# Kernel tuning notes

Measured on AMD Instinct MI355X. Metric: run time of the kernel, lower is better.

The kernel has to match this reference:

```python
import jax, jax.numpy as jnp
import numpy as np

N, E = 2048, 262144
SDIM, VDIM, EDIM = 256, 64, 32
NUM_ATOM_FEATURES, NUM_BOND_TYPES, NMOL = 16, 5, 64


def setup_inputs() -> dict:
    key = jax.random.key(0)
    ks = jax.random.split(key, 18)
    def lin(k, fan_in, shape):
        return jax.random.uniform(k, shape, jnp.float32, -1.0, 1.0) / np.sqrt(fan_in)
    inp = {
        "s": jax.random.normal(ks[0], (N, SDIM), jnp.float32),
        "v": jax.random.normal(ks[1], (N, 3, VDIM), jnp.float32),
        "p": jax.random.normal(ks[2], (N, 3), jnp.float32),
        "e": jax.random.normal(ks[3], (E, EDIM), jnp.float32),
        "batch": jnp.sort(jax.random.randint(ks[4], (N,), 0, NMOL)),
        "edge_index_global": jax.random.randint(ks[5], (2, E), 0, N),
        # learned params (torch DenseLayer == Linear): W [in,out], b [out]
        "Ws": lin(ks[6], SDIM, (SDIM, SDIM)),   "bs": lin(ks[7], SDIM, (SDIM,)),
        "Wc": lin(ks[8], VDIM, (VDIM, 1)),                                      # coords_lin, no bias
        "Wa": lin(ks[9], SDIM, (SDIM, NUM_ATOM_FEATURES)), "ba": lin(ks[10], SDIM, (NUM_ATOM_FEATURES,)),
        "Wb": lin(ks[11], EDIM, (EDIM, SDIM)),  "bb": lin(ks[12], EDIM, (SDIM,)),
        "W0": lin(ks[13], SDIM + 1, (SDIM + 1, SDIM)), "b0": lin(ks[14], SDIM + 1, (SDIM,)),
        "W1": lin(ks[15], SDIM, (SDIM, NUM_BOND_TYPES)), "b1": lin(ks[16], SDIM, (NUM_BOND_TYPES,)),
    }
    return inp


def reference(s, v, p, e, batch, edge_index_global,
              Ws, bs, Wc, Wa, ba, Wb, bb, W0, b0, W1, b1):
    # shared scalar mapping with SiLU
    s_h = jax.nn.silu(s @ Ws + bs)                              # [N, SDIM]
    coords = (v @ Wc)[..., 0]                                   # [N,3,VDIM]@[VDIM,1] -> [N,3]
    atoms_pred = s_h @ Wa + ba                                  # [N, NUM_ATOM_FEATURES]

    j, i = edge_index_global[0], edge_index_global[1]
    # coords_param == 'data': add positions then remove per-graph mean (scatter_mean)
    coords_pred = p + coords
    sums = jax.ops.segment_sum(coords_pred, batch, num_segments=NMOL)       # [NMOL,3]
    cnts = jax.ops.segment_sum(jnp.ones((N, 1), s.dtype), batch, num_segments=NMOL)
    coords_pred = coords_pred - (sums / jnp.maximum(cnts, 1.0))[batch]

    d = jnp.sum((coords_pred[i] - coords_pred[j]) ** 2, axis=-1, keepdims=True)  # [E,1]

    # dense edge matrix construction + symmetrization (as in the original)
    e_dense = jnp.zeros((N, N, EDIM), e.dtype).at[j, i].set(e)  # [N,N,EDIM]
    e_dense = 0.5 * (e_dense + jnp.swapaxes(e_dense, 0, 1))
    e_sym = e_dense[j, i]                                        # [E,EDIM]

    f = s_h[i] + s_h[j] + (e_sym @ Wb + bb)                      # [E,SDIM]
    edge = jnp.concatenate([f, d], axis=-1)                      # [E,SDIM+1]
    bonds_pred = jax.nn.silu(edge @ W0 + b0) @ W1 + b1           # [E,NUM_BOND_TYPES]
    return coords_pred, atoms_pred, bonds_pred
```

## Files before the change

kernel.cpp:

```cpp
#include <hip/hip_runtime.h>
#include <hip/hip_bf16.h>

typedef __bf16 bf16_8 __attribute__((ext_vector_type(8)));
typedef __bf16 bf16_4 __attribute__((ext_vector_type(4)));
typedef float f32x4 __attribute__((ext_vector_type(4)));

__device__ __forceinline__ float silu_f(float x) {
    return x * __builtin_amdgcn_rcpf(1.0f + __expf(-x));
}

__device__ __forceinline__ unsigned hslot(unsigned cell, unsigned nslots) {
    return (unsigned)(((unsigned long long)(cell * 2654435761u) * nslots) >> 32);
}
__device__ __forceinline__ int map_lookup(unsigned nslots, const int* __restrict__ M,
                                          const unsigned long long* __restrict__ H, unsigned cell) {
    if (nslots == 0) return M[cell] - 1;
    unsigned slot = hslot(cell, nslots);
    for (int pr = 0; pr < 4096; pr++) {
        unsigned long long v = H[slot];
        if (v == 0ull) return -1;
        if ((unsigned)(v >> 32) == cell) return (int)(v & 0xFFFFFFFFu) - 1;
        slot++; if (slot == nslots) slot = 0;
    }
    return -1;
}

__global__ __launch_bounds__(256) void kS(float* __restrict__ out, int n, float val) {
    int i = blockIdx.x * 256 + threadIdx.x;
    if (i < n) out[i] = val;
}

__global__ __launch_bounds__(256) void kZ(f32x4* __restrict__ a, size_t na16,
                                          f32x4* __restrict__ b, size_t nb16) {
    size_t i = (size_t)blockIdx.x * 256 + threadIdx.x;
    size_t stride = (size_t)gridDim.x * 256;
    f32x4 z = {0.f, 0.f, 0.f, 0.f};
    for (size_t k = i; k < na16; k += stride) a[k] = z;
    for (size_t k = i; k < nb16; k += stride) b[k] = z;
}

__global__ __launch_bounds__(256, 4) void kP(
    const float* __restrict__ s, const float* __restrict__ Ws, const float* __restrict__ bs,
    const float* __restrict__ W0, const float* __restrict__ Wa, const float* __restrict__ ba,
    const float* __restrict__ v, const float* __restrict__ p,
    const float* __restrict__ Wc, const float* __restrict__ Wb, const float* __restrict__ bb,
    const float* __restrict__ b0, const float* __restrict__ W1,
    const int* __restrict__ batch, const int* __restrict__ ei,
    int N, int E, int gaB, int coordB, int mapB,
    unsigned nslots, int* __restrict__ M, unsigned long long* __restrict__ H,
    __bf16* __restrict__ G, __bf16* __restrict__ wqT, __bf16* __restrict__ w1Tg,
    float* __restrict__ w0L, float* __restrict__ b0p,
    float* __restrict__ cp, float* __restrict__ sums, float* __restrict__ cnts,
    float* __restrict__ outA)
{
    __shared__ __align__(16) char LDSC[37376];
    int b = blockIdx.x, t = threadIdx.x;

    if (b < gaB) {
        __bf16* s_bf  = (__bf16*)LDSC;
        __bf16* sh_bf = (__bf16*)(LDSC + 8448);
        __bf16* wT    = (__bf16*)(LDSC + 16896);
        int wv = t >> 6, lane = t & 63;
        int l16 = lane & 15, q8 = (lane >> 4) * 8, r4b = (lane >> 4) * 4;
        int r0 = b * 16;
        {
            int row = t >> 4, c0 = (t & 15) * 16;
            const float* sp = s + (long long)(r0 + row) * 256 + c0;
            bool ok = (r0 + row) < N;
            f32x4 a0 = ok ? *(const f32x4*)(sp + 0)  : (f32x4){0.f,0.f,0.f,0.f};
            f32x4 a1 = ok ? *(const f32x4*)(sp + 4)  : (f32x4){0.f,0.f,0.f,0.f};
            f32x4 a2 = ok ? *(const f32x4*)(sp + 8)  : (f32x4){0.f,0.f,0.f,0.f};
            f32x4 a3 = ok ? *(const f32x4*)(sp + 12) : (f32x4){0.f,0.f,0.f,0.f};
            bf16_8 p0, p1;
#pragma unroll
            for (int q = 0; q < 4; q++) {
                p0[q] = (__bf16)a0[q]; p0[q + 4] = (__bf16)a1[q];
                p1[q] = (__bf16)a2[q]; p1[q + 4] = (__bf16)a3[q];
            }
            *(bf16_8*)(s_bf + row * 264 + c0) = p0;
            *(bf16_8*)(s_bf + row * 264 + c0 + 8) = p1;
        }
        __syncthreads();
        __bf16* wTw = wT + wv * 2560;
        float ld[32];

        f32x4 acc[4];
#pragma unroll
        for (int ct = 0; ct < 4; ct++) acc[ct] = (f32x4){0.f,0.f,0.f,0.f};
        {
            const float* wp = Ws + wv * 64 + lane;
#pragma unroll
            for (int i = 0; i < 32; i++) ld[i] = wp[i * 256];
#pragma unroll 1
            for (int kk = 0; kk < 8; kk++) {
#pragma unroll
                for (int j = 0; j < 4; j++) {
                    bf16_8 pk;
#pragma unroll
                    for (int q = 0; q < 8; q++) pk[q] = (__bf16)ld[j * 8 + q];
                    *(bf16_8*)(wTw + lane * 40 + j * 8) = pk;
                }
                if (kk < 7) {
                    const float* wpn = wp + (kk + 1) * 32 * 256;
#pragma unroll
                    for (int i = 0; i < 32; i++) ld[i] = wpn[i * 256];
                }
                bf16_8 af = *(const bf16_8*)(s_bf + l16 * 264 + kk * 32 + q8);
#pragma unroll
                for (int ct = 0; ct < 4; ct++) {
                    bf16_8 bfr = *(const bf16_8*)(wTw + (ct * 16 + l16) * 40 + q8);
                    acc[ct] = __builtin_amdgcn_mfma_f32_16x16x32_bf16(af, bfr, acc[ct], 0, 0, 0);
                }
            }
        }
#pragma unroll
        for (int ct = 0; ct < 4; ct++) {
            int col = wv * 64 + ct * 16 + l16;
            float bsv = bs[col];
#pragma unroll
            for (int r = 0; r < 4; r++)
                sh_bf[(r4b + r) * 264 + col] = (__bf16)silu_f(acc[ct][r] + bsv);
        }
        __syncthreads();

        if (wv == 0) {
            f32x4 aa = (f32x4){0.f,0.f,0.f,0.f};
#pragma unroll 1
            for (int ks = 0; ks < 8; ks++) {
                bf16_8 a = *(const bf16_8*)(sh_bf + l16 * 264 + ks * 32 + q8);
                bf16_8 wb;
#pragma unroll
                for (int j = 0; j < 8; j++) wb[j] = (__bf16)Wa[(ks * 32 + q8 + j) * 16 + l16];
                aa = __builtin_amdgcn_mfma_f32_16x16x32_bf16(a, wb, aa, 0, 0, 0);
            }
            float bav = ba[l16];
#pragma unroll
            for (int r = 0; r < 4; r++) {
                int row = r0 + r4b + r;
                if (row < N) outA[row * 16 + l16] = aa[r] + bav;
            }
        }

        f32x4 acc2[4];
#pragma unroll
        for (int ct = 0; ct < 4; ct++) acc2[ct] = (f32x4){0.f,0.f,0.f,0.f};
        {
            const float* wp = W0 + wv * 64 + lane;
#pragma unroll
            for (int i = 0; i < 32; i++) ld[i] = wp[i * 256];
#pragma unroll 1
            for (int kk = 0; kk < 8; kk++) {
#pragma unroll
                for (int j = 0; j < 4; j++) {
                    bf16_8 pk;
#pragma unroll
                    for (int q = 0; q < 8; q++) pk[q] = (__bf16)ld[j * 8 + q];
                    *(bf16_8*)(wTw + lane * 40 + j * 8) = pk;
                }
                if (kk < 7) {
                    const float* wpn = wp + (kk + 1) * 32 * 256;
#pragma unroll
                    for (int i = 0; i < 32; i++) ld[i] = wpn[i * 256];
                }
                bf16_8 af = *(const bf16_8*)(sh_bf + l16 * 264 + kk * 32 + q8);
#pragma unroll
                for (int ct = 0; ct < 4; ct++) {
                    bf16_8 bfr = *(const bf16_8*)(wTw + (ct * 16 + l16) * 40 + q8);
                    acc2[ct] = __builtin_amdgcn_mfma_f32_16x16x32_bf16(af, bfr, acc2[ct], 0, 0, 0);
                }
            }
        }
#pragma unroll
        for (int ct = 0; ct < 4; ct++) {
            int col = wv * 64 + ct * 16 + l16;
#pragma unroll
            for (int r = 0; r < 4; r++) {
                int row = r0 + r4b + r;
                if (row < N) G[(long long)row * 256 + col] = (__bf16)acc2[ct][r];
            }
        }
        return;
    }
    b -= gaB;

    float* sm = (float*)LDSC;
    if (b < 2) {
        int r0 = b * 16;
        for (int i4 = t; i4 < 1024; i4 += 256)
            ((f32x4*)sm)[i4] = ((const f32x4*)(Wb + r0 * 256))[i4];
        __syncthreads();
        float acc[16];
#pragma unroll
        for (int r = 0; r < 16; r++) acc[r] = 0.f;
        for (int m4 = 0; m4 < 64; m4++) {
            float w0v = W0[(m4 * 4 + 0) * 256 + t];
            float w1v = W0[(m4 * 4 + 1) * 256 + t];
            float w2v = W0[(m4 * 4 + 2) * 256 + t];
            float w3v = W0[(m4 * 4 + 3) * 256 + t];
#pragma unroll
            for (int r = 0; r < 16; r++) {
                f32x4 sv = *(const f32x4*)(sm + r * 256 + m4 * 4);
                acc[r] += sv[0] * w0v + sv[1] * w1v + sv[2] * w2v + sv[3] * w3v;
            }
        }
#pragma unroll
        for (int r = 0; r < 16; r++) wqT[t * 32 + r0 + r] = (__bf16)acc[r];
        return;
    }
    b -= 2;
    if (b < 1) {
        sm[t] = bb[t];
        __syncthreads();
        float acc = 0.f;
        for (int m4 = 0; m4 < 64; m4++) {
            f32x4 bv = *(const f32x4*)(sm + m4 * 4);
            acc += bv[0] * W0[(m4 * 4 + 0) * 256 + t] + bv[1] * W0[(m4 * 4 + 1) * 256 + t]
                 + bv[2] * W0[(m4 * 4 + 2) * 256 + t] + bv[3] * W0[(m4 * 4 + 3) * 256 + t];
        }
        b0p[t] = acc + b0[t];
        w0L[t] = W0[256 * 256 + t];
#pragma unroll
        for (int c = 0; c < 16; c++)
            w1Tg[c * 256 + t] = (c < 5) ? (__bf16)W1[t * 5 + c] : (__bf16)0.f;
        return;
    }
    b -= 1;
    if (b < coordB) {
        int n = b * 256 + t;
        if (t < 64) sm[t] = Wc[t];
        __syncthreads();
        if (n < N) {
            int mb = batch[n] & 1023;
#pragma unroll
            for (int ax = 0; ax < 3; ax++) {
                float acc = 0.f;
                for (int d4 = 0; d4 < 16; d4++) {
                    f32x4 vv = *(const f32x4*)(v + (long long)n * 192 + ax * 64 + d4 * 4);
                    f32x4 wv2 = *(const f32x4*)(sm + d4 * 4);
                    acc += vv[0] * wv2[0] + vv[1] * wv2[1] + vv[2] * wv2[2] + vv[3] * wv2[3];
                }
                float val = p[n * 3 + ax] + acc;
                cp[n * 3 + ax] = val;
                atomicAdd(&sums[mb * 3 + ax], val);
            }
            atomicAdd(&cnts[mb], 1.0f);
        }
        return;
    }
    b -= coordB;
    {
        int k = b * 256 + t;
        if (k < E) {
            int jj = ei[k], ii = ei[E + k];
            if ((unsigned)jj >= (unsigned)N) jj = 0;
            if ((unsigned)ii >= (unsigned)N) ii = 0;
            unsigned cell = (unsigned)jj * (unsigned)N + (unsigned)ii;
            if (nslots == 0) {
                atomicMax(&M[cell], k + 1);
            } else {
                unsigned long long mine = ((unsigned long long)cell << 32) | (unsigned)(k + 1);
                unsigned slot = hslot(cell, nslots);
                for (int pr = 0; pr < 4096; pr++) {
                    unsigned long long old = atomicCAS(&H[slot], 0ull, mine);
                    if (old == 0ull) break;
                    if ((unsigned)(old >> 32) == cell) { atomicMax(&H[slot], mine); break; }
                    slot++; if (slot == nslots) slot = 0;
                }
            }
        }
    }
}

__global__ __launch_bounds__(256, 4) void kC(
    const float* __restrict__ e, const int* __restrict__ ei, const int* __restrict__ batch,
    int N, int E, int edgeB, unsigned nslots,
    const int* __restrict__ M, const unsigned long long* __restrict__ H,
    const __bf16* __restrict__ G, const __bf16* __restrict__ wqTg,
    const __bf16* __restrict__ w1Tg,
    const float* __restrict__ w0L, const float* __restrict__ b0p,
    const float* __restrict__ cp, const float* __restrict__ sums, const float* __restrict__ cnts,
    const float* __restrict__ b1,
    float* __restrict__ outC, float* __restrict__ bonds)
{
    if (blockIdx.x >= (unsigned)edgeB) {
        int n = ((int)blockIdx.x - edgeB) * 256 + threadIdx.x;
        if (n < N) {
            int mb = batch[n] & 1023;
            float cnt = fmaxf(cnts[mb], 1.0f);
#pragma unroll
            for (int ax = 0; ax < 3; ax++)
                outC[n * 3 + ax] = cp[n * 3 + ax] - sums[mb * 3 + ax] / cnt;
        }
        return;
    }

    __shared__ __align__(16) __bf16 esym[64 * 40];
    __shared__ __align__(16) __bf16 hbuf[64 * 264];
    __shared__ float sd[64];
    __shared__ int si[64], sj[64], sm1[64], sm2[64];

    int t = threadIdx.x;
    int wv = t >> 6, lane = t & 63;
    int l16 = lane & 15, q8 = (lane >> 4) * 8;
    int e0 = blockIdx.x * 64;

    if (t < 128) {
        int tt = t & 63;
        int k = e0 + tt;
        if (t < 64) {
            if (k >= E) {
                si[tt] = 0; sj[tt] = 0; sm1[tt] = 0; sd[tt] = 0.f;
            } else {
                int jj = ei[k], ii = ei[E + k];
                if ((unsigned)jj >= (unsigned)N) jj = 0;
                if ((unsigned)ii >= (unsigned)N) ii = 0;
                si[tt] = ii; sj[tt] = jj;
                int m1 = map_lookup(nslots, M, H, (unsigned)jj * (unsigned)N + (unsigned)ii);
                sm1[tt] = ((unsigned)m1 < (unsigned)E) ? m1 : 0;
                int bi = batch[ii] & 1023, bj = batch[jj] & 1023;
                float inv_i = __builtin_amdgcn_rcpf(fmaxf(cnts[bi], 1.0f));
                float inv_j = __builtin_amdgcn_rcpf(fmaxf(cnts[bj], 1.0f));
                float dx = (cp[ii * 3 + 0] - sums[bi * 3 + 0] * inv_i) - (cp[jj * 3 + 0] - sums[bj * 3 + 0] * inv_j);
                float dy = (cp[ii * 3 + 1] - sums[bi * 3 + 1] * inv_i) - (cp[jj * 3 + 1] - sums[bj * 3 + 1] * inv_j);
                float dz = (cp[ii * 3 + 2] - sums[bi * 3 + 2] * inv_i) - (cp[jj * 3 + 2] - sums[bj * 3 + 2] * inv_j);
                sd[tt] = dx * dx + dy * dy + dz * dz;
            }
        } else {
            if (k >= E) {
                sm2[tt] = -1;
            } else {
                int jj = ei[k], ii = ei[E + k];
                if ((unsigned)jj >= (unsigned)N) jj = 0;
                if ((unsigned)ii >= (unsigned)N) ii = 0;
                int m2 = map_lookup(nslots, M, H, (unsigned)ii * (unsigned)N + (unsigned)jj);
                sm2[tt] = ((unsigned)m2 < (unsigned)E) ? m2 : -1;
            }
        }
    }
    __syncthreads();

    {
        int er = t >> 2, qg = (t & 3) * 8;
        int m1 = sm1[er], m2 = sm2[er];
        const float* e1p = e + (size_t)m1 * 32 + qg;
        float v1[8], v2[8];
#pragma unroll
        for (int q = 0; q < 8; q++) { v1[q] = e1p[q]; v2[q] = 0.f; }
        if (m2 >= 0) {
            const float* e2p = e + (size_t)m2 * 32 + qg;
#pragma unroll
            for (int q = 0; q < 8; q++) v2[q] = e2p[q];
        }
        bf16_8 es;
#pragma unroll
        for (int q = 0; q < 8; q++) es[q] = (__bf16)(0.5f * (v1[q] + v2[q]));
        *(bf16_8*)(esym + er * 40 + qg) = es;
    }
    {
        int c4 = lane * 4;
        for (int it = 0; it < 16; it++) {
            int er = wv * 16 + it;
            bf16_4 gi = *(const bf16_4*)(G + (size_t)si[er] * 256 + c4);
            bf16_4 gj = *(const bf16_4*)(G + (size_t)sj[er] * 256 + c4);
            bf16_4 o;
#pragma unroll
            for (int q = 0; q < 4; q++) o[q] = (__bf16)((float)gi[q] + (float)gj[q]);
            *(bf16_4*)(hbuf + er * 264 + c4) = o;
        }
    }
    __syncthreads();

    f32x4 acc[4][4];
#pragma unroll
    for (int rt = 0; rt < 4; rt++)
#pragma unroll
        for (int ct = 0; ct < 4; ct++)
            acc[rt][ct] = (f32x4){0.f, 0.f, 0.f, 0.f};
    bf16_8 af[4];
#pragma unroll
    for (int rt = 0; rt < 4; rt++)
        af[rt] = *(const bf16_8*)(esym + (rt * 16 + l16) * 40 + q8);
#pragma unroll
    for (int ct = 0; ct < 4; ct++) {
        int c = (wv * 4 + ct) * 16 + l16;
        bf16_8 bfr = *(const bf16_8*)(wqTg + c * 32 + q8);
#pragma unroll
        for (int rt = 0; rt < 4; rt++)
            acc[rt][ct] = __builtin_amdgcn_mfma_f32_16x16x32_bf16(af[rt], bfr, acc[rt][ct], 0, 0, 0);
    }
    int r4base = (lane >> 4) * 4;
    f32x4 sdv[4];
#pragma unroll
    for (int rt = 0; rt < 4; rt++)
        sdv[rt] = *(const f32x4*)(sd + rt * 16 + r4base);
#pragma unroll
    for (int ct = 0; ct < 4; ct++) {
        int col = (wv * 4 + ct) * 16 + l16;
        float w0c = w0L[col], b0c = b0p[col];
#pragma unroll
        for (int rt = 0; rt < 4; rt++) {
#pragma unroll
            for (int r4 = 0; r4 < 4; r4++) {
                int row = rt * 16 + r4base + r4;
                int off = row * 264 + col;
                float x = acc[rt][ct][r4] + b0c + sdv[rt][r4] * w0c + (float)hbuf[off];
                hbuf[off] = (__bf16)silu_f(x);
            }
        }
    }
    __syncthreads();

    f32x4 acc3 = {0.f, 0.f, 0.f, 0.f};
#pragma unroll
    for (int ks = 0; ks < 8; ks++) {
        bf16_8 a = *(const bf16_8*)(hbuf + (wv * 16 + l16) * 264 + ks * 32 + q8);
        bf16_8 b2 = *(const bf16_8*)(w1Tg + l16 * 256 + ks * 32 + q8);
        acc3 = __builtin_amdgcn_mfma_f32_16x16x32_bf16(a, b2, acc3, 0, 0, 0);
    }
    if (l16 < 5) {
        float bv = b1[l16];
#pragma unroll
        for (int r4 = 0; r4 < 4; r4++) {
            int row = wv * 16 + r4base + r4;
            if (e0 + row < E)
                bonds[(size_t)(e0 + row) * 5 + l16] = acc3[r4] + bv;
        }
    }
}

extern "C" void kernel_launch(void* const* d_in, const int* in_sizes, int n_in,
                              void* d_out, int out_size, void* d_ws, size_t ws_size,
                              hipStream_t stream)
{
    const float* s  = (const float*)d_in[0];
    const float* v  = (const float*)d_in[1];
    const float* p  = (const float*)d_in[2];
    const float* e  = (const float*)d_in[3];
    const int* batch = (const int*)d_in[4];
    const int* ei    = (const int*)d_in[5];
    const float* Ws = (const float*)d_in[6];
    const float* bs = (const float*)d_in[7];
    const float* Wc = (const float*)d_in[8];
    const float* Wa = (const float*)d_in[9];
    const float* ba = (const float*)d_in[10];
    const float* Wb = (const float*)d_in[11];
    const float* bb = (const float*)d_in[12];
    const float* W0 = (const float*)d_in[13];
    const float* b0 = (const float*)d_in[14];
    const float* W1 = (const float*)d_in[15];
    const float* b1 = (const float*)d_in[16];

    float* out = (float*)d_out;
    int sentN = out_size < 8192 ? out_size : 8192;

    int N = in_sizes[0] / 256;
    long long E = in_sizes[5] / 2;
    int code = 0;
    if (in_sizes[6] != 65536) code |= 1;
    if (in_sizes[8] != 64) code |= 2;
    if (in_sizes[11] != 32 * 256) code |= 4;
    if (in_sizes[9] != 16 * 256) code |= 8;
    if (in_sizes[15] != 5 * 256) code |= 16;
    if (in_sizes[13] != 257 * 256) code |= 32;
    if (N < 1 || in_sizes[0] != N * 256) code |= 64;
    if (in_sizes[1] != (long long)N * 192) code |= 128;
    if (in_sizes[2] != N * 3) code |= 256;
    if (in_sizes[3] != E * 32) code |= 512;
    if (in_sizes[4] != N) code |= 1024;
    if ((long long)out_size != 19LL * N + 5LL * E) code |= 2048;
    if (code) {
        kS<<<(sentN + 255) / 256, 256, 0, stream>>>(out, sentN, 3000.0f + 64.0f * (float)code);
        return;
    }
    int Ei = (int)E;

    auto align256 = [](size_t x) { return (x + 255) & ~(size_t)255; };
    size_t G_b  = align256((size_t)N * 512);
    size_t cp_b = align256((size_t)N * 12);
    size_t misc = G_b + 16384 + 8192 + 1024 + 1024 + cp_b + 12288 + 4096 + 256;
    size_t denseB = (size_t)N * (size_t)N * 4;
    unsigned nslots; size_t mapBytes;
    if (ws_size >= denseB + misc) {
        nslots = 0; mapBytes = denseB;
    } else {
        size_t avail = (ws_size > misc) ? (ws_size - misc) / 8 : 0;
        size_t want = (size_t)Ei * 2;
        size_t ns = avail < want ? avail : want;
        if (ns < (size_t)Ei + (size_t)Ei / 8) {
            unsigned mb = (unsigned)(ws_size >> 20); if (mb > 120) mb = 120;
            kS<<<(sentN + 255) / 256, 256, 0, stream>>>(out, sentN, 1000.0f + 8.0f * (float)mb);
            return;
        }
        nslots = (unsigned)ns; mapBytes = ns * 8;
    }

    char* ws = (char*)d_ws;
    int* M = (int*)ws;
    unsigned long long* H = (unsigned long long*)ws;
    size_t mapZ = align256(mapBytes);
    size_t off = mapZ;
    __bf16* G    = (__bf16*)(ws + off); off += G_b;
    __bf16* wqT  = (__bf16*)(ws + off); off += 16384;
    __bf16* w1Tg = (__bf16*)(ws + off); off += 8192;
    float* w0L  = (float*)(ws + off);  off += 1024;
    float* b0p  = (float*)(ws + off);  off += 1024;
    float* cp   = (float*)(ws + off);  off += cp_b;
    float* sums = (float*)(ws + off);  off += 12288;
    float* cnts = (float*)(ws + off);  off += 4096;

    float* outC = out;
    float* outA = outC + 3 * N;
    float* outB = outC + 19 * N;

    kZ<<<2048, 256, 0, stream>>>((f32x4*)ws, mapZ >> 4, (f32x4*)sums, 1024);

    int mapB = (Ei + 255) / 256;
    int coordB = (N + 255) / 256;
    int gaB = (N + 15) / 16;
    kP<<<gaB + 3 + coordB + mapB, 256, 0, stream>>>(
        s, Ws, bs, W0, Wa, ba, v, p, Wc, Wb, bb, b0, W1, batch, ei,
        N, Ei, gaB, coordB, mapB, nslots, M, H,
        G, wqT, w1Tg, w0L, b0p, cp, sums, cnts, outA);
    int edgeB = (Ei + 63) / 64;
    kC<<<edgeB + coordB, 256, 0, stream>>>(
        e, ei, batch, N, Ei, edgeB, nslots, M, H, G, wqT, w1Tg,
        w0L, b0p, cp, sums, cnts, b1, outC, outB);
}
```

Measured before the change: 194.8 us.

## Pre-transpose weights to bf16 and halve edge-kernel LDS for occupancy

The zero-fill kernel now also converts Ws, W0 and Wa into transposed bf16 copies in workspace. The node kernel therefore reads MFMA B-fragments straight from global memory instead of staging converted weights through LDS, and its LDS footprint drops. The Wb·W0 product is moved onto MFMA. The edge kernel processes the 256 hidden columns in two halves through a 64x136 LDS buffer, which roughly halves its LDS use, and raises its launch bound to 6 blocks. In exchange it gathers G twice and adds extra barriers.

Result: slower. 267.4 us (+37.3%).

```diff
diff --git a/kernel.cpp b/kernel.cpp
--- a/kernel.cpp
+++ b/kernel.cpp
@@ -30,21 +30,49 @@
     if (i < n) out[i] = val;
 }
 
-__global__ __launch_bounds__(256) void kZ(f32x4* __restrict__ a, size_t na16,
-                                          f32x4* __restrict__ b, size_t nb16) {
-    size_t i = (size_t)blockIdx.x * 256 + threadIdx.x;
-    size_t stride = (size_t)gridDim.x * 256;
+__global__ __launch_bounds__(256) void kZ(
+    f32x4* __restrict__ a, size_t na16, f32x4* __restrict__ b, size_t nb16,
+    const float* __restrict__ Ws, const float* __restrict__ W0, const float* __restrict__ Wa,
+    __bf16* __restrict__ WsT, __bf16* __restrict__ W0T, __bf16* __restrict__ WaT)
+{
+    int bid = blockIdx.x, t = threadIdx.x;
+    if (bid < 4) {
+        for (int idx = t; idx < 64 * 256; idx += 256) {
+            int kl = idx >> 8, c = idx & 255;
+            WsT[(size_t)c * 256 + bid * 64 + kl] = (__bf16)Ws[(size_t)(bid * 64 + kl) * 256 + c];
+        }
+        return;
+    }
+    bid -= 4;
+    if (bid < 4) {
+        for (int idx = t; idx < 64 * 256; idx += 256) {
+            int kl = idx >> 8, c = idx & 255;
+            W0T[(size_t)c * 256 + bid * 64 + kl] = (__bf16)W0[(size_t)(bid * 64 + kl) * 256 + c];
+        }
+        return;
+    }
+    bid -= 4;
+    if (bid < 1) {
+        for (int idx = t; idx < 4096; idx += 256) {
+            int k = idx >> 4, c = idx & 15;
+            WaT[c * 256 + k] = (__bf16)Wa[k * 16 + c];
+        }
+        return;
+    }
+    bid -= 1;
+    size_t i = (size_t)bid * 256 + t;
+    size_t stride = (size_t)(gridDim.x - 9) * 256;
     f32x4 z = {0.f, 0.f, 0.f, 0.f};
     for (size_t k = i; k < na16; k += stride) a[k] = z;
     for (size_t k = i; k < nb16; k += stride) b[k] = z;
 }
 
 __global__ __launch_bounds__(256, 4) void kP(
-    const float* __restrict__ s, const float* __restrict__ Ws, const float* __restrict__ bs,
-    const float* __restrict__ W0, const float* __restrict__ Wa, const float* __restrict__ ba,
+    const float* __restrict__ s, const float* __restrict__ bs, const float* __restrict__ ba,
+    const __bf16* __restrict__ WsT, const __bf16* __restrict__ W0T, const __bf16* __restrict__ WaT,
     const float* __restrict__ v, const float* __restrict__ p,
     const float* __restrict__ Wc, const float* __restrict__ Wb, const float* __restrict__ bb,
-    const float* __restrict__ b0, const float* __restrict__ W1,
+    const float* __restrict__ W0, const float* __restrict__ b0, const float* __restrict__ W1,
     const int* __restrict__ batch, const int* __restrict__ ei,
     int N, int E, int gaB, int coordB, int mapB,
     unsigned nslots, int* __restrict__ M, unsigned long long* __restrict__ H,
@@ -53,15 +81,15 @@
     float* __restrict__ cp, float* __restrict__ sums, float* __restrict__ cnts,
     float* __restrict__ outA)
 {
-    __shared__ __align__(16) char LDSC[37376];
+    __shared__ __align__(16) char LDSC[16896];
+    __bf16* s_bf  = (__bf16*)LDSC;
+    __bf16* sh_bf = (__bf16*)(LDSC + 8448);
+    float* sm = (float*)LDSC;
     int b = blockIdx.x, t = threadIdx.x;
+    int wv = t >> 6, lane = t & 63;
+    int l16 = lane & 15, q8 = (lane >> 4) * 8, r4b = (lane >> 4) * 4;
 
     if (b < gaB) {
-        __bf16* s_bf  = (__bf16*)LDSC;
-        __bf16* sh_bf = (__bf16*)(LDSC + 8448);
-        __bf16* wT    = (__bf16*)(LDSC + 16896);
-        int wv = t >> 6, lane = t & 63;
-        int l16 = lane & 15, q8 = (lane >> 4) * 8, r4b = (lane >> 4) * 4;
         int r0 = b * 16;
         {
             int row = t >> 4, c0 = (t & 15) * 16;
@@ -73,44 +101,25 @@
             f32x4 a3 = ok ? *(const f32x4*)(sp + 12) : (f32x4){0.f,0.f,0.f,0.f};
             bf16_8 p0, p1;
 #pragma unroll
-            for (int q = 0; q < 4; q++) {
-                p0[q] = (__bf16)a0[q]; p0[q + 4] = (__bf16)a1[q];
-                p1[q] = (__bf16)a2[q]; p1[q + 4] = (__bf16)a3[q];
+            for (int qq = 0; qq < 4; qq++) {
+                p0[qq] = (__bf16)a0[qq]; p0[qq + 4] = (__bf16)a1[qq];
+                p1[qq] = (__bf16)a2[qq]; p1[qq + 4] = (__bf16)a3[qq];
             }
             *(bf16_8*)(s_bf + row * 264 + c0) = p0;
             *(bf16_8*)(s_bf + row * 264 + c0 + 8) = p1;
         }
         __syncthreads();
-        __bf16* wTw = wT + wv * 2560;
-        float ld[32];
 
         f32x4 acc[4];
 #pragma unroll
         for (int ct = 0; ct < 4; ct++) acc[ct] = (f32x4){0.f,0.f,0.f,0.f};
-        {
-            const float* wp = Ws + wv * 64 + lane;
-#pragma unroll
-            for (int i = 0; i < 32; i++) ld[i] = wp[i * 256];
-#pragma unroll 1
-            for (int kk = 0; kk < 8; kk++) {
-#pragma unroll
-                for (int j = 0; j < 4; j++) {
-                    bf16_8 pk;
-#pragma unroll
-                    for (int q = 0; q < 8; q++) pk[q] = (__bf16)ld[j * 8 + q];
-                    *(bf16_8*)(wTw + lane * 40 + j * 8) = pk;
-                }
-                if (kk < 7) {
-                    const float* wpn = wp + (kk + 1) * 32 * 256;
-#pragma unroll
-                    for (int i = 0; i < 32; i++) ld[i] = wpn[i * 256];
-                }
-                bf16_8 af = *(const bf16_8*)(s_bf + l16 * 264 + kk * 32 + q8);
-#pragma unroll
-                for (int ct = 0; ct < 4; ct++) {
-                    bf16_8 bfr = *(const bf16_8*)(wTw + (ct * 16 + l16) * 40 + q8);
-                    acc[ct] = __builtin_amdgcn_mfma_f32_16x16x32_bf16(af, bfr, acc[ct], 0, 0, 0);
-                }
+#pragma unroll
+        for (int kk = 0; kk < 8; kk++) {
+            bf16_8 af = *(const bf16_8*)(s_bf + l16 * 264 + kk * 32 + q8);
+#pragma unroll
+            for (int ct = 0; ct < 4; ct++) {
+                bf16_8 bw = *(const bf16_8*)(WsT + (size_t)(wv * 64 + ct * 16 + l16) * 256 + kk * 32 + q8);
+                acc[ct] = __builtin_amdgcn_mfma_f32_16x16x32_bf16(af, bw, acc[ct], 0, 0, 0);
             }
         }
 #pragma unroll
@@ -125,13 +134,11 @@
 
         if (wv == 0) {
             f32x4 aa = (f32x4){0.f,0.f,0.f,0.f};
-#pragma unroll 1
+#pragma unroll
             for (int ks = 0; ks < 8; ks++) {
-                bf16_8 a = *(const bf16_8*)(sh_bf + l16 * 264 + ks * 32 + q8);
-                bf16_8 wb;
-#pragma unroll
-                for (int j = 0; j < 8; j++) wb[j] = (__bf16)Wa[(ks * 32 + q8 + j) * 16 + l16];
-                aa = __builtin_amdgcn_mfma_f32_16x16x32_bf16(a, wb, aa, 0, 0, 0);
+                bf16_8 af = *(const bf16_8*)(sh_bf + l16 * 264 + ks * 32 + q8);
+                bf16_8 bw = *(const bf16_8*)(WaT + (size_t)l16 * 256 + ks * 32 + q8);
+                aa = __builtin_amdgcn_mfma_f32_16x16x32_bf16(af, bw, aa, 0, 0, 0);
             }
             float bav = ba[l16];
 #pragma unroll
@@ -144,30 +151,13 @@
         f32x4 acc2[4];
 #pragma unroll
         for (int ct = 0; ct < 4; ct++) acc2[ct] = (f32x4){0.f,0.f,0.f,0.f};
-        {
-            const float* wp = W0 + wv * 64 + lane;
-#pragma unroll
-            for (int i = 0; i < 32; i++) ld[i] = wp[i * 256];
-#pragma unroll 1
-            for (int kk = 0; kk < 8; kk++) {
-#pragma unroll
-                for (int j = 0; j < 4; j++) {
-                    bf16_8 pk;
-#pragma unroll
-                    for (int q = 0; q < 8; q++) pk[q] = (__bf16)ld[j * 8 + q];
-                    *(bf16_8*)(wTw + lane * 40 + j * 8) = pk;
-                }
-                if (kk < 7) {
-                    const float* wpn = wp + (kk + 1) * 32 * 256;
-#pragma unroll
-                    for (int i = 0; i < 32; i++) ld[i] = wpn[i * 256];
-                }
-                bf16_8 af = *(const bf16_8*)(sh_bf + l16 * 264 + kk * 32 + q8);
-#pragma unroll
-                for (int ct = 0; ct < 4; ct++) {
-                    bf16_8 bfr = *(const bf16_8*)(wTw + (ct * 16 + l16) * 40 + q8);
-                    acc2[ct] = __builtin_amdgcn_mfma_f32_16x16x32_bf16(af, bfr, acc2[ct], 0, 0, 0);
-                }
+#pragma unroll
+        for (int kk = 0; kk < 8; kk++) {
+            bf16_8 af = *(const bf16_8*)(sh_bf + l16 * 264 + kk * 32 + q8);
+#pragma unroll
+            for (int ct = 0; ct < 4; ct++) {
+                bf16_8 bw = *(const bf16_8*)(W0T + (size_t)(wv * 64 + ct * 16 + l16) * 256 + kk * 32 + q8);
+                acc2[ct] = __builtin_amdgcn_mfma_f32_16x16x32_bf16(af, bw, acc2[ct], 0, 0, 0);
             }
         }
 #pragma unroll
@@ -183,28 +173,44 @@
     }
     b -= gaB;
 
-    float* sm = (float*)LDSC;
     if (b < 2) {
         int r0 = b * 16;
-        for (int i4 = t; i4 < 1024; i4 += 256)
-            ((f32x4*)sm)[i4] = ((const f32x4*)(Wb + r0 * 256))[i4];
+        {
+            int row = t >> 4, c0 = (t & 15) * 16;
+            const float* wp = Wb + (long long)(r0 + row) * 256 + c0;
+            f32x4 a0 = *(const f32x4*)(wp + 0);
+            f32x4 a1 = *(const f32x4*)(wp + 4);
+            f32x4 a2 = *(const f32x4*)(wp + 8);
+            f32x4 a3 = *(const f32x4*)(wp + 12);
+            bf16_8 p0, p1;
+#pragma unroll
+            for (int qq = 0; qq < 4; qq++) {
+                p0[qq] = (__bf16)a0[qq]; p0[qq + 4] = (__bf16)a1[qq];
+                p1[qq] = (__bf16)a2[qq]; p1[qq + 4] = (__bf16)a3[qq];
+            }
+            *(bf16_8*)(s_bf + row * 264 + c0) = p0;
+            *(bf16_8*)(s_bf + row * 264 + c0 + 8) = p1;
+        }
         __syncthreads();
-        float acc[16];
-#pragma unroll
-        for (int r = 0; r < 16; r++) acc[r] = 0.f;
-        for (int m4 = 0; m4 < 64; m4++) {
-            float w0v = W0[(m4 * 4 + 0) * 256 + t];
-            float w1v = W0[(m4 * 4 + 1) * 256 + t];
-            float w2v = W0[(m4 * 4 + 2) * 256 + t];
-            float w3v = W0[(m4 * 4 + 3) * 256 + t];
-#pragma unroll
-            for (int r = 0; r < 16; r++) {
-                f32x4 sv = *(const f32x4*)(sm + r * 256 + m4 * 4);
-                acc[r] += sv[0] * w0v + sv[1] * w1v + sv[2] * w2v + sv[3] * w3v;
-            }
-        }
-#pragma unroll
-        for (int r = 0; r < 16; r++) wqT[t * 32 + r0 + r] = (__bf16)acc[r];
+        f32x4 acc[4];
+#pragma unroll
+        for (int ct = 0; ct < 4; ct++) acc[ct] = (f32x4){0.f,0.f,0.f,0.f};
+#pragma unroll
+        for (int kk = 0; kk < 8; kk++) {
+            bf16_8 af = *(const bf16_8*)(s_bf + l16 * 264 + kk * 32 + q8);
+#pragma unroll
+            for (int ct = 0; ct < 4; ct++) {
+                bf16_8 bw = *(const bf16_8*)(W0T + (size_t)(wv * 64 + ct * 16 + l16) * 256 + kk * 32 + q8);
+                acc[ct] = __builtin_amdgcn_mfma_f32_16x16x32_bf16(af, bw, acc[ct], 0, 0, 0);
+            }
+        }
+#pragma unroll
+        for (int ct = 0; ct < 4; ct++) {
+            int col = wv * 64 + ct * 16 + l16;
+#pragma unroll
+            for (int r = 0; r < 4; r++)
+                wqT[col * 32 + r0 + r4b + r] = (__bf16)acc[ct][r];
+        }
         return;
     }
     b -= 2;
@@ -271,7 +277,7 @@
     }
 }
 
-__global__ __launch_bounds__(256, 4) void kC(
+__global__ __launch_bounds__(256, 6) void kC(
     const float* __restrict__ e, const int* __restrict__ ei, const int* __restrict__ batch,
     int N, int E, int edgeB, unsigned nslots,
     const int* __restrict__ M, const unsigned long long* __restrict__ H,
@@ -295,13 +301,13 @@
     }
 
     __shared__ __align__(16) __bf16 esym[64 * 40];
-    __shared__ __align__(16) __bf16 hbuf[64 * 264];
+    __shared__ __align__(16) __bf16 hb[64 * 136];
     __shared__ float sd[64];
     __shared__ int si[64], sj[64], sm1[64], sm2[64];
 
     int t = threadIdx.x;
     int wv = t >> 6, lane = t & 63;
-    int l16 = lane & 15, q8 = (lane >> 4) * 8;
+    int l16 = lane & 15, q8 = (lane >> 4) * 8, r4b = (lane >> 4) * 4;
     int e0 = blockIdx.x * 64;
 
     if (t < 128) {
@@ -345,27 +351,30 @@
         const float* e1p = e + (size_t)m1 * 32 + qg;
         float v1[8], v2[8];
 #pragma unroll
-        for (int q = 0; q < 8; q++) { v1[q] = e1p[q]; v2[q] = 0.f; }
+        for (int qq = 0; qq < 8; qq++) { v1[qq] = e1p[qq]; v2[qq] = 0.f; }
         if (m2 >= 0) {
             const float* e2p = e + (size_t)m2 * 32 + qg;
 #pragma unroll
-            for (int q = 0; q < 8; q++) v2[q] = e2p[q];
+            for (int qq = 0; qq < 8; qq++) v2[qq] = e2p[qq];
         }
         bf16_8 es;
 #pragma unroll
-        for (int q = 0; q < 8; q++) es[q] = (__bf16)(0.5f * (v1[q] + v2[q]));
+        for (int qq = 0; qq < 8; qq++) es[qq] = (__bf16)(0.5f * (v1[qq] + v2[qq]));
         *(bf16_8*)(esym + er * 40 + qg) = es;
     }
     {
-        int c4 = lane * 4;
-        for (int it = 0; it < 16; it++) {
-            int er = wv * 16 + it;
-            bf16_4 gi = *(const bf16_4*)(G + (size_t)si[er] * 256 + c4);
-            bf16_4 gj = *(const bf16_4*)(G + (size_t)sj[er] * 256 + c4);
-            bf16_4 o;
-#pragma unroll
-            for (int q = 0; q < 4; q++) o[q] = (__bf16)((float)gi[q] + (float)gj[q]);
-            *(bf16_4*)(hbuf + er * 264 + c4) = o;
+        int er = t >> 2, qd = t & 3;
+        const __bf16* Gi = G + (size_t)si[er] * 256 + qd * 64;
+        const __bf16* Gj = G + (size_t)sj[er] * 256 + qd * 64;
+        __bf16* dst = hb + er * 136 + qd * 32;
+#pragma unroll
+        for (int h8 = 0; h8 < 4; h8++) {
+            bf16_8 gi = *(const bf16_8*)(Gi + h8 * 8);
+            bf16_8 gj = *(const bf16_8*)(Gj + h8 * 8);
+            bf16_8 o;
+#pragma unroll
+            for (int qq = 0; qq < 8; qq++) o[qq] = (__bf16)((float)gi[qq] + (float)gj[qq]);
+            *(bf16_8*)(dst + h8 * 8) = o;
         }
     }
     __syncthreads();
@@ -382,29 +391,28 @@
         af[rt] = *(const bf16_8*)(esym + (rt * 16 + l16) * 40 + q8);
 #pragma unroll
     for (int ct = 0; ct < 4; ct++) {
-        int c = (wv * 4 + ct) * 16 + l16;
+        int c = wv * 64 + ct * 16 + l16;
         bf16_8 bfr = *(const bf16_8*)(wqTg + c * 32 + q8);
 #pragma unroll
         for (int rt = 0; rt < 4; rt++)
             acc[rt][ct] = __builtin_amdgcn_mfma_f32_16x16x32_bf16(af[rt], bfr, acc[rt][ct], 0, 0, 0);
     }
-    int r4base = (lane >> 4) * 4;
     f32x4 sdv[4];
 #pragma unroll
     for (int rt = 0; rt < 4; rt++)
-        sdv[rt] = *(const f32x4*)(sd + rt * 16 + r4base);
-#pragma unroll
-    for (int ct = 0; ct < 4; ct++) {
-        int col = (wv * 4 + ct) * 16 + l16;
+        sdv[rt] = *(const f32x4*)(sd + rt * 16 + r4b);
+#pragma unroll
+    for (int ct = 0; ct < 2; ct++) {
+        int col = wv * 64 + ct * 16 + l16;
+        int scol = wv * 32 + ct * 16 + l16;
         float w0c = w0L[col], b0c = b0p[col];
 #pragma unroll
         for (int rt = 0; rt < 4; rt++) {
 #pragma unroll
             for (int r4 = 0; r4 < 4; r4++) {
-                int row = rt * 16 + r4base + r4;
-                int off = row * 264 + col;
-                float x = acc[rt][ct][r4] + b0c + sdv[rt][r4] * w0c + (float)hbuf[off];
-                hbuf[off] = (__bf16)silu_f(x);
+                int off = (rt * 16 + r4b + r4) * 136 + scol;
+                float x = acc[rt][ct][r4] + b0c + sdv[rt][r4] * w0c + (float)hb[off];
+                hb[off] = (__bf16)silu_f(x);
             }
         }
     }
@@ -412,16 +420,58 @@
 
     f32x4 acc3 = {0.f, 0.f, 0.f, 0.f};
 #pragma unroll
-    for (int ks = 0; ks < 8; ks++) {
-        bf16_8 a = *(const bf16_8*)(hbuf + (wv * 16 + l16) * 264 + ks * 32 + q8);
-        bf16_8 b2 = *(const bf16_8*)(w1Tg + l16 * 256 + ks * 32 + q8);
+    for (int kp = 0; kp < 4; kp++) {
+        bf16_8 a = *(const bf16_8*)(hb + (wv * 16 + l16) * 136 + kp * 32 + q8);
+        bf16_8 b2 = *(const bf16_8*)(w1Tg + l16 * 256 + (kp * 2) * 32 + q8);
+        acc3 = __builtin_amdgcn_mfma_f32_16x16x32_bf16(a, b2, acc3, 0, 0, 0);
+    }
+    __syncthreads();
+
+    {
+        int er = t >> 2, qd = t & 3;
+        const __bf16* Gi = G + (size_t)si[er] * 256 + qd * 64 + 32;
+        const __bf16* Gj = G + (size_t)sj[er] * 256 + qd * 64 + 32;
+        __bf16* dst = hb + er * 136 + qd * 32;
+#pragma unroll
+        for (int h8 = 0; h8 < 4; h8++) {
+            bf16_8 gi = *(const bf16_8*)(Gi + h8 * 8);
+            bf16_8 gj = *(const bf16_8*)(Gj + h8 * 8);
+            bf16_8 o;
+#pragma unroll
+            for (int qq = 0; qq < 8; qq++) o[qq] = (__bf16)((float)gi[qq] + (float)gj[qq]);
+            *(bf16_8*)(dst + h8 * 8) = o;
+        }
+    }
+    __syncthreads();
+
+#pragma unroll
+    for (int ct = 2; ct < 4; ct++) {
+        int col = wv * 64 + ct * 16 + l16;
+        int scol = wv * 32 + (ct - 2) * 16 + l16;
+        float w0c = w0L[col], b0c = b0p[col];
+#pragma unroll
+        for (int rt = 0; rt < 4; rt++) {
+#pragma unroll
+            for (int r4 = 0; r4 < 4; r4++) {
+                int off = (rt * 16 + r4b + r4) * 136 + scol;
+                float x = acc[rt][ct][r4] + b0c + sdv[rt][r4] * w0c + (float)hb[off];
+                hb[off] = (__bf16)silu_f(x);
+            }
+        }
+    }
+    __syncthreads();
+
+#pragma unroll
+    for (int kp = 0; kp < 4; kp++) {
+        bf16_8 a = *(const bf16_8*)(hb + (wv * 16 + l16) * 136 + kp * 32 + q8);
+        bf16_8 b2 = *(const bf16_8*)(w1Tg + l16 * 256 + (kp * 2 + 1) * 32 + q8);
         acc3 = __builtin_amdgcn_mfma_f32_16x16x32_bf16(a, b2, acc3, 0, 0, 0);
     }
     if (l16 < 5) {
         float bv = b1[l16];
 #pragma unroll
         for (int r4 = 0; r4 < 4; r4++) {
-            int row = wv * 16 + r4base + r4;
+            int row = wv * 16 + r4b + r4;
             if (e0 + row < E)
                 bonds[(size_t)(e0 + row) * 5 + l16] = acc3[r4] + bv;
         }
@@ -477,7 +527,8 @@
     auto align256 = [](size_t x) { return (x + 255) & ~(size_t)255; };
     size_t G_b  = align256((size_t)N * 512);
     size_t cp_b = align256((size_t)N * 12);
-    size_t misc = G_b + 16384 + 8192 + 1024 + 1024 + cp_b + 12288 + 4096 + 256;
+    size_t misc = G_b + 16384 + 8192 + 131072 + 131072 + 8192
+                + 1024 + 1024 + cp_b + 12288 + 4096 + 256;
     size_t denseB = (size_t)N * (size_t)N * 4;
     unsigned nslots; size_t mapBytes;
     if (ws_size >= denseB + misc) {
@@ -502,6 +553,9 @@
     __bf16* G    = (__bf16*)(ws + off); off += G_b;
     __bf16* wqT  = (__bf16*)(ws + off); off += 16384;
     __bf16* w1Tg = (__bf16*)(ws + off); off += 8192;
+    __bf16* WsT  = (__bf16*)(ws + off); off += 131072;
+    __bf16* W0T  = (__bf16*)(ws + off); off += 131072;
+    __bf16* WaT  = (__bf16*)(ws + off); off += 8192;
     float* w0L  = (float*)(ws + off);  off += 1024;
     float* b0p  = (float*)(ws + off);  off += 1024;
     float* cp   = (float*)(ws + off);  off += cp_b;
@@ -512,13 +566,15 @@
     float* outA = outC + 3 * N;
     float* outB = outC + 19 * N;
 
-    kZ<<<2048, 256, 0, stream>>>((f32x4*)ws, mapZ >> 4, (f32x4*)sums, 1024);
+    kZ<<<9 + 2048, 256, 0, stream>>>(
+        (f32x4*)ws, mapZ >> 4, (f32x4*)sums, 1024,
+        Ws, W0, Wa, WsT, W0T, WaT);
 
     int mapB = (Ei + 255) / 256;
     int coordB = (N + 255) / 256;
     int gaB = (N + 15) / 16;
     kP<<<gaB + 3 + coordB + mapB, 256, 0, stream>>>(
-        s, Ws, bs, W0, Wa, ba, v, p, Wc, Wb, bb, b0, W1, batch, ei,
+        s, bs, ba, WsT, W0T, WaT, v, p, Wc, Wb, bb, W0, b0, W1, batch, ei,
         N, Ei, gaB, coordB, mapB, nslots, M, H,
         G, wqT, w1Tg, w0L, b0p, cp, sums, cnts, outA);
     int edgeB = (Ei + 63) / 64;
```

## Drop dense N×N edge map in favor of compact hash map always

Applied to the files above, without the earlier changes.

Removes the dense N*N int index map path, which required zeroing 16 MB of workspace and scattering into it, and always uses the open-addressing hash table sized to about 2E slots. This shrinks the zero-fill and the random-access footprint of the map. In exchange, inserts and lookups now do CAS-based linear probing. The edge kernel is also reordered so the MFMA result is written to LDS first and the gathered G rows are added with SiLU afterwards, and the zero-fill grid is reduced.

Measured after the change: 211.7 us. 1.09x slower.

```diff
diff --git a/kernel.cpp b/kernel.cpp
--- a/kernel.cpp
+++ b/kernel.cpp
@@ -12,9 +12,8 @@
 __device__ __forceinline__ unsigned hslot(unsigned cell, unsigned nslots) {
     return (unsigned)(((unsigned long long)(cell * 2654435761u) * nslots) >> 32);
 }
-__device__ __forceinline__ int map_lookup(unsigned nslots, const int* __restrict__ M,
+__device__ __forceinline__ int map_lookup(unsigned nslots,
                                           const unsigned long long* __restrict__ H, unsigned cell) {
-    if (nslots == 0) return M[cell] - 1;
     unsigned slot = hslot(cell, nslots);
     for (int pr = 0; pr < 4096; pr++) {
         unsigned long long v = H[slot];
@@ -47,7 +46,7 @@
     const float* __restrict__ b0, const float* __restrict__ W1,
     const int* __restrict__ batch, const int* __restrict__ ei,
     int N, int E, int gaB, int coordB, int mapB,
-    unsigned nslots, int* __restrict__ M, unsigned long long* __restrict__ H,
+    unsigned nslots, unsigned long long* __restrict__ H,
     __bf16* __restrict__ G, __bf16* __restrict__ wqT, __bf16* __restrict__ w1Tg,
     float* __restrict__ w0L, float* __restrict__ b0p,
     float* __restrict__ cp, float* __restrict__ sums, float* __restrict__ cnts,
@@ -255,17 +254,13 @@
             if ((unsigned)jj >= (unsigned)N) jj = 0;
             if ((unsigned)ii >= (unsigned)N) ii = 0;
             unsigned cell = (unsigned)jj * (unsigned)N + (unsigned)ii;
-            if (nslots == 0) {
-                atomicMax(&M[cell], k + 1);
-            } else {
-                unsigned long long mine = ((unsigned long long)cell << 32) | (unsigned)(k + 1);
-                unsigned slot = hslot(cell, nslots);
-                for (int pr = 0; pr < 4096; pr++) {
-                    unsigned long long old = atomicCAS(&H[slot], 0ull, mine);
-                    if (old == 0ull) break;
-                    if ((unsigned)(old >> 32) == cell) { atomicMax(&H[slot], mine); break; }
-                    slot++; if (slot == nslots) slot = 0;
-                }
+            unsigned long long mine = ((unsigned long long)cell << 32) | (unsigned)(k + 1);
+            unsigned slot = hslot(cell, nslots);
+            for (int pr = 0; pr < 4096; pr++) {
+                unsigned long long old = atomicCAS(&H[slot], 0ull, mine);
+                if (old == 0ull) break;
+                if ((unsigned)(old >> 32) == cell) { atomicMax(&H[slot], mine); break; }
+                slot++; if (slot == nslots) slot = 0;
             }
         }
     }
@@ -274,7 +269,7 @@
 __global__ __launch_bounds__(256, 4) void kC(
     const float* __restrict__ e, const int* __restrict__ ei, const int* __restrict__ batch,
     int N, int E, int edgeB, unsigned nslots,
-    const int* __restrict__ M, const unsigned long long* __restrict__ H,
+    const unsigned long long* __restrict__ H,
     const __bf16* __restrict__ G, const __bf16* __restrict__ wqTg,
     const __bf16* __restrict__ w1Tg,
     const float* __restrict__ w0L, const float* __restrict__ b0p,
@@ -301,7 +296,7 @@
 
     int t = threadIdx.x;
     int wv = t >> 6, lane = t & 63;
-    int l16 = lane & 15, q8 = (lane >> 4) * 8;
+    int l16 = lane & 15, q8 = (lane >> 4) * 8, r4b = (lane >> 4) * 4;
     int e0 = blockIdx.x * 64;
 
     if (t < 128) {
@@ -315,7 +310,7 @@
                 if ((unsigned)jj >= (unsigned)N) jj = 0;
                 if ((unsigned)ii >= (unsigned)N) ii = 0;
                 si[tt] = ii; sj[tt] = jj;
-                int m1 = map_lookup(nslots, M, H, (unsigned)jj * (unsigned)N + (unsigned)ii);
+                int m1 = map_lookup(nslots, H, (unsigned)jj * (unsigned)N + (unsigned)ii);
                 sm1[tt] = ((unsigned)m1 < (unsigned)E) ? m1 : 0;
                 int bi = batch[ii] & 1023, bj = batch[jj] & 1023;
                 float inv_i = __builtin_amdgcn_rcpf(fmaxf(cnts[bi], 1.0f));
@@ -332,7 +327,7 @@
                 int jj = ei[k], ii = ei[E + k];
                 if ((unsigned)jj >= (unsigned)N) jj = 0;
                 if ((unsigned)ii >= (unsigned)N) ii = 0;
-                int m2 = map_lookup(nslots, M, H, (unsigned)ii * (unsigned)N + (unsigned)jj);
+                int m2 = map_lookup(nslots, H, (unsigned)ii * (unsigned)N + (unsigned)jj);
                 sm2[tt] = ((unsigned)m2 < (unsigned)E) ? m2 : -1;
             }
         }
@@ -356,59 +351,62 @@
         for (int q = 0; q < 8; q++) es[q] = (__bf16)(0.5f * (v1[q] + v2[q]));
         *(bf16_8*)(esym + er * 40 + qg) = es;
     }
+    __syncthreads();
+
+    f32x4 acc[4][4];
+#pragma unroll
+    for (int rt = 0; rt < 4; rt++)
+#pragma unroll
+        for (int ct = 0; ct < 4; ct++)
+            acc[rt][ct] = (f32x4){0.f, 0.f, 0.f, 0.f};
+    bf16_8 af[4];
+#pragma unroll
+    for (int rt = 0; rt < 4; rt++)
+        af[rt] = *(const bf16_8*)(esym + (rt * 16 + l16) * 40 + q8);
+#pragma unroll
+    for (int ct = 0; ct < 4; ct++) {
+        int c = (wv * 4 + ct) * 16 + l16;
+        bf16_8 bfr = *(const bf16_8*)(wqTg + c * 32 + q8);
+#pragma unroll
+        for (int rt = 0; rt < 4; rt++)
+            acc[rt][ct] = __builtin_amdgcn_mfma_f32_16x16x32_bf16(af[rt], bfr, acc[rt][ct], 0, 0, 0);
+    }
+    f32x4 sdv[4];
+#pragma unroll
+    for (int rt = 0; rt < 4; rt++)
+        sdv[rt] = *(const f32x4*)(sd + rt * 16 + r4b);
+#pragma unroll
+    for (int ct = 0; ct < 4; ct++) {
+        int col = (wv * 4 + ct) * 16 + l16;
+        float w0c = w0L[col], b0c = b0p[col];
+#pragma unroll
+        for (int rt = 0; rt < 4; rt++) {
+#pragma unroll
+            for (int r4 = 0; r4 < 4; r4++) {
+                int row = rt * 16 + r4b + r4;
+                hbuf[row * 264 + col] = (__bf16)(acc[rt][ct][r4] + b0c + sdv[rt][r4] * w0c);
+            }
+        }
+    }
+    __syncthreads();
+
     {
         int c4 = lane * 4;
         for (int it = 0; it < 16; it++) {
             int er = wv * 16 + it;
-            bf16_4 gi = *(const bf16_4*)(G + (size_t)si[er] * 256 + c4);
-            bf16_4 gj = *(const bf16_4*)(G + (size_t)sj[er] * 256 + c4);
+            int ii = si[er], jj = sj[er];
+            bf16_4 gi = *(const bf16_4*)(G + (size_t)ii * 256 + c4);
+            bf16_4 gj = *(const bf16_4*)(G + (size_t)jj * 256 + c4);
+            bf16_4 hv = *(const bf16_4*)(hbuf + er * 264 + c4);
             bf16_4 o;
 #pragma unroll
-            for (int q = 0; q < 4; q++) o[q] = (__bf16)((float)gi[q] + (float)gj[q]);
+            for (int q = 0; q < 4; q++) {
+                float x = (float)hv[q] + (float)gi[q] + (float)gj[q];
+                o[q] = (__bf16)silu_f(x);
+            }
             *(bf16_4*)(hbuf + er * 264 + c4) = o;
         }
     }
-    __syncthreads();
-
-    f32x4 acc[4][4];
-#pragma unroll
-    for (int rt = 0; rt < 4; rt++)
-#pragma unroll
-        for (int ct = 0; ct < 4; ct++)
-            acc[rt][ct] = (f32x4){0.f, 0.f, 0.f, 0.f};
-    bf16_8 af[4];
-#pragma unroll
-    for (int rt = 0; rt < 4; rt++)
-        af[rt] = *(const bf16_8*)(esym + (rt * 16 + l16) * 40 + q8);
-#pragma unroll
-    for (int ct = 0; ct < 4; ct++) {
-        int c = (wv * 4 + ct) * 16 + l16;
-        bf16_8 bfr = *(const bf16_8*)(wqTg + c * 32 + q8);
-#pragma unroll
-        for (int rt = 0; rt < 4; rt++)
-            acc[rt][ct] = __builtin_amdgcn_mfma_f32_16x16x32_bf16(af[rt], bfr, acc[rt][ct], 0, 0, 0);
-    }
-    int r4base = (lane >> 4) * 4;
-    f32x4 sdv[4];
-#pragma unroll
-    for (int rt = 0; rt < 4; rt++)
-        sdv[rt] = *(const f32x4*)(sd + rt * 16 + r4base);
-#pragma unroll
-    for (int ct = 0; ct < 4; ct++) {
-        int col = (wv * 4 + ct) * 16 + l16;
-        float w0c = w0L[col], b0c = b0p[col];
-#pragma unroll
-        for (int rt = 0; rt < 4; rt++) {
-#pragma unroll
-            for (int r4 = 0; r4 < 4; r4++) {
-                int row = rt * 16 + r4base + r4;
-                int off = row * 264 + col;
-                float x = acc[rt][ct][r4] + b0c + sdv[rt][r4] * w0c + (float)hbuf[off];
-                hbuf[off] = (__bf16)silu_f(x);
-            }
-        }
-    }
-    __syncthreads();
 
     f32x4 acc3 = {0.f, 0.f, 0.f, 0.f};
 #pragma unroll
@@ -421,7 +419,7 @@
         float bv = b1[l16];
 #pragma unroll
         for (int r4 = 0; r4 < 4; r4++) {
-            int row = wv * 16 + r4base + r4;
+            int row = wv * 16 + r4b + r4;
             if (e0 + row < E)
                 bonds[(size_t)(e0 + row) * 5 + l16] = acc3[r4] + bv;
         }
@@ -478,24 +476,19 @@
     size_t G_b  = align256((size_t)N * 512);
     size_t cp_b = align256((size_t)N * 12);
     size_t misc = G_b + 16384 + 8192 + 1024 + 1024 + cp_b + 12288 + 4096 + 256;
-    size_t denseB = (size_t)N * (size_t)N * 4;
-    unsigned nslots; size_t mapBytes;
-    if (ws_size >= denseB + misc) {
-        nslots = 0; mapBytes = denseB;
-    } else {
-        size_t avail = (ws_size > misc) ? (ws_size - misc) / 8 : 0;
-        size_t want = (size_t)Ei * 2;
-        size_t ns = avail < want ? avail : want;
-        if (ns < (size_t)Ei + (size_t)Ei / 8) {
-            unsigned mb = (unsigned)(ws_size >> 20); if (mb > 120) mb = 120;
-            kS<<<(sentN + 255) / 256, 256, 0, stream>>>(out, sentN, 1000.0f + 8.0f * (float)mb);
-            return;
-        }
-        nslots = (unsigned)ns; mapBytes = ns * 8;
-    }
+
+    size_t avail = (ws_size > misc) ? (ws_size - misc) / 8 : 0;
+    size_t want = (size_t)Ei * 2;
+    size_t ns = avail < want ? avail : want;
+    if (ns < (size_t)Ei + (size_t)Ei / 8) {
+        unsigned mb = (unsigned)(ws_size >> 20); if (mb > 120) mb = 120;
+        kS<<<(sentN + 255) / 256, 256, 0, stream>>>(out, sentN, 1000.0f + 8.0f * (float)mb);
+        return;
+    }
+    unsigned nslots = (unsigned)ns;
+    size_t mapBytes = ns * 8;
 
     char* ws = (char*)d_ws;
-    int* M = (int*)ws;
     unsigned long long* H = (unsigned long long*)ws;
     size_t mapZ = align256(mapBytes);
     size_t off = mapZ;
@@ -512,17 +505,17 @@
     float* outA = outC + 3 * N;
     float* outB = outC + 19 * N;
 
-    kZ<<<2048, 256, 0, stream>>>((f32x4*)ws, mapZ >> 4, (f32x4*)sums, 1024);
+    kZ<<<512, 256, 0, stream>>>((f32x4*)ws, mapZ >> 4, (f32x4*)sums, 1024);
 
     int mapB = (Ei + 255) / 256;
     int coordB = (N + 255) / 256;
     int gaB = (N + 15) / 16;
     kP<<<gaB + 3 + coordB + mapB, 256, 0, stream>>>(
         s, Ws, bs, W0, Wa, ba, v, p, Wc, Wb, bb, b0, W1, batch, ei,
-        N, Ei, gaB, coordB, mapB, nslots, M, H,
+        N, Ei, gaB, coordB, mapB, nslots, H,
         G, wqT, w1Tg, w0L, b0p, cp, sums, cnts, outA);
     int edgeB = (Ei + 63) / 64;
     kC<<<edgeB + coordB, 256, 0, stream>>>(
-        e, ei, batch, N, Ei, edgeB, nslots, M, H, G, wqT, w1Tg,
+        e, ei, batch, N, Ei, edgeB, nslots, H, G, wqT, w1Tg,
         w0L, b0p, cp, sums, cnts, b1, outC, outB);
 }
```
